# Performance work log

Measured on AMD Instinct MI355X. Metric: run time of the kernel, lower is better.

Reference implementation:

```python
import jax, jax.numpy as jnp
import numpy as np


def kernel_mus(n_kernels):
    l_mu = [1.0]
    if n_kernels == 1:
        return l_mu
    bin_size = 2.0 / (n_kernels - 1)
    l_mu.append(1 - bin_size / 2)
    for i in range(1, n_kernels - 1):
        l_mu.append(l_mu[i] - bin_size)
    return l_mu


def kernel_sigmas(n_kernels):
    bin_size = 2.0 / (n_kernels - 1)
    l_sigma = [0.0001]
    if n_kernels == 1:
        return l_sigma
    l_sigma += [0.5 * bin_size] * (n_kernels - 1)
    return l_sigma


def setup_inputs() -> dict:
    key = jax.random.key(0)
    k0, k1, k2, k3 = jax.random.split(key, 4)
    B, Q, D, E, V, K = 256, 32, 512, 300, 100000, 11
    query_tokens = jax.random.randint(k0, (B, Q), 0, V)
    doc_tokens = jax.random.randint(k1, (B, D), 0, V)
    emb_table = jax.random.normal(k2, (V, E), jnp.float32) * 0.02
    dense_w = jax.random.uniform(k3, (1, K), jnp.float32, -0.014, 0.014)
    dense_b = jnp.zeros((1,), jnp.float32)
    mu = jnp.asarray(kernel_mus(K), jnp.float32)
    sigma = jnp.asarray(kernel_sigmas(K), jnp.float32)
    return {"query_tokens": query_tokens, "doc_tokens": doc_tokens,
            "emb_table": emb_table, "dense_w": dense_w, "dense_b": dense_b,
            "mu": mu, "sigma": sigma}


def reference(query_tokens, doc_tokens, emb_table, dense_w, dense_b, mu, sigma):
    EPS = 1e-13  # CosineMatrixAttention tiny value
    q_mask = (query_tokens > 0).astype(jnp.float32)   # [B,Q]
    d_mask = (doc_tokens > 0).astype(jnp.float32)     # [B,D]
    q_emb = emb_table[query_tokens]                   # [B,Q,E]
    d_emb = emb_table[doc_tokens]                     # [B,D,E]
    q_n = q_emb / (jnp.linalg.norm(q_emb, axis=-1, keepdims=True) + EPS)
    d_n = d_emb / (jnp.linalg.norm(d_emb, axis=-1, keepdims=True) + EPS)
    cosine = jnp.einsum('bqe,bde->bqd', q_n, d_n)     # [B,Q,D]
    pair_mask = q_mask[:, :, None] * d_mask[:, None, :]  # [B,Q,D]
    cosine_masked = cosine * pair_mask
    # gaussian kernels: [B,Q,D,K]
    diff = cosine_masked[..., None] - mu
    kernels = jnp.exp(-(diff * diff) / (2.0 * sigma * sigma)) * pair_mask[..., None]
    per_kernel_query = jnp.sum(kernels, axis=2)       # [B,Q,K]
    log_pkq = jnp.log(jnp.clip(per_kernel_query, 1e-10)) * 0.01
    log_pkq = log_pkq * q_mask[..., None]
    per_kernel = jnp.sum(log_pkq, axis=1)             # [B,K]
    out = per_kernel @ dense_w.T + dense_b            # [B,1]
    return out[:, 0]
```

## Files before the change

### kernel.cpp

```cpp
#include <hip/hip_runtime.h>


#define B      256
#define BQ     32
#define BD     512
#define EDIM   300
#define KPAD   320
#define NK     11
#define DTILE  64
#define NCHUNK 16
#define DSTR   324

typedef float floatx4 __attribute__((ext_vector_type(4)));
typedef short shortx8 __attribute__((ext_vector_type(8)));

__device__ __forceinline__ unsigned short f2bf(float f) {
    unsigned int u = __float_as_uint(f);
    return (unsigned short)((u + 0x7fffu + ((u >> 16) & 1u)) >> 16);
}
__device__ __forceinline__ float bf2f(unsigned short h) {
    return __uint_as_float(((unsigned int)h) << 16);
}

__global__ __launch_bounds__(256)
void knrm_norm(const float* __restrict__ emb, unsigned short* __restrict__ ebf,
               float* __restrict__ rnorm, int V)
{
    int r    = blockIdx.x * 16 + (threadIdx.x >> 4);
    int part = threadIdx.x & 15;
    if (r >= V) return;
    const float4* src = (const float4*)(emb + (size_t)r * EDIM);
    uint2*        dst = (uint2*)(ebf + (size_t)r * KPAD);
    float ss = 0.f;
    #pragma unroll
    for (int i = 0; i < 5; ++i) {
        int c = part + i * 16;
        uint2 p = {0u, 0u};
        if (c < EDIM / 4) {
            float4 v = src[c];
            unsigned short h0 = f2bf(v.x), h1 = f2bf(v.y), h2 = f2bf(v.z), h3 = f2bf(v.w);
            p.x = (unsigned int)h0 | ((unsigned int)h1 << 16);
            p.y = (unsigned int)h2 | ((unsigned int)h3 << 16);
            float f0 = bf2f(h0), f1 = bf2f(h1), f2 = bf2f(h2), f3 = bf2f(h3);
            ss += f0 * f0 + f1 * f1 + f2 * f2 + f3 * f3;
        }
        dst[c] = p;
    }
    ss += __shfl_xor(ss, 1);
    ss += __shfl_xor(ss, 2);
    ss += __shfl_xor(ss, 4);
    ss += __shfl_xor(ss, 8);
    if (part == 0) rnorm[r] = 1.f / (sqrtf(ss) + 1e-13f);
}

__global__ __launch_bounds__(256)
void knrm_main3(const int* __restrict__ qtok, const int* __restrict__ dtok,
                const unsigned short* __restrict__ ebf, const float* __restrict__ rnorm,
                const float* __restrict__ mu, const float* __restrict__ sigma,
                float* __restrict__ pkq_part)
{
    __shared__ unsigned short d_buf[DTILE * DSTR];

    const int tid   = threadIdx.x;
    const int lane  = tid & 63;
    const int wv    = tid >> 6;
    const int b     = blockIdx.x >> 3;
    const int g     = blockIdx.x & 7;
    const int l16   = lane & 15;
    const int quad  = lane >> 4;
    const int mbase = (wv & 1) * 16;
    const int sub   = wv >> 1;
    const int nbase = sub * 32;
    const int chunk = g * 2 + sub;

    const int tq  = qtok[b * BQ + mbase + l16];
    const int td0 = dtok[b * BD + g * DTILE + nbase + l16];
    const int td1 = dtok[b * BD + g * DTILE + nbase + 16 + l16];
    float rq  = rnorm[tq];
    float rd0 = rnorm[td0], dm0 = (td0 > 0) ? 1.f : 0.f;
    float rd1 = rnorm[td1], dm1 = (td1 > 0) ? 1.f : 0.f;

    const uint4* asrc = (const uint4*)(ebf + (size_t)tq * KPAD);
    shortx8 afrag[10];
    #pragma unroll
    for (int ks = 0; ks < 10; ++ks)
        afrag[ks] = *(const shortx8*)&asrc[quad + ks * 4];

    float mur[NK], cfr[NK];
    #pragma unroll
    for (int k = 0; k < NK; ++k) {
        float s = sigma[k];
        mur[k] = mu[k];
        cfr[k] = -0.5f / (s * s);
    }

    {
        int row = tid >> 2, part = tid & 3;
        int tok = dtok[b * BD + g * DTILE + row];
        const uint4* src = (const uint4*)(ebf + (size_t)tok * KPAD);
        #pragma unroll
        for (int i = 0; i < 10; ++i) {
            int c = part + i * 4;
            *(uint4*)&d_buf[row * DSTR + c * 8] = src[c];
        }
    }
    __syncthreads();

    const unsigned short* b0ptr = &d_buf[(nbase + l16) * DSTR + quad * 8];
    const unsigned short* b1ptr = b0ptr + 16 * DSTR;

    floatx4 acc0 = {0.f, 0.f, 0.f, 0.f};
    floatx4 acc1 = {0.f, 0.f, 0.f, 0.f};
    #pragma unroll
    for (int ks = 0; ks < 10; ++ks) {
        shortx8 b0 = *(const shortx8*)(b0ptr + ks * 32);
        shortx8 b1 = *(const shortx8*)(b1ptr + ks * 32);
        acc0 = __builtin_amdgcn_mfma_f32_16x16x32_bf16(afrag[ks], b0, acc0, 0, 0, 0);
        acc1 = __builtin_amdgcn_mfma_f32_16x16x32_bf16(afrag[ks], b1, acc1, 0, 0, 0);
    }

    float rqv[4];
    #pragma unroll
    for (int r = 0; r < 4; ++r) rqv[r] = __shfl(rq, quad * 4 + r);

    float* dst = pkq_part + (size_t)(b * NCHUNK + chunk) * (BQ * NK);
    #pragma unroll
    for (int r = 0; r < 4; ++r) {
        float c0 = acc0[r] * rqv[r] * rd0;
        float c1 = acc1[r] * rqv[r] * rd1;
        int q = mbase + quad * 4 + r;
        #pragma unroll
        for (int k = 0; k < NK; ++k) {
            float d0 = c0 - mur[k];
            float d1 = c1 - mur[k];
            float v = dm0 * __expf(cfr[k] * d0 * d0)
                    + dm1 * __expf(cfr[k] * d1 * d1);
            v += __shfl_xor(v, 1);
            v += __shfl_xor(v, 2);
            v += __shfl_xor(v, 4);
            v += __shfl_xor(v, 8);
            if (l16 == 0) dst[q * NK + k] = v;
        }
    }
}

__global__ __launch_bounds__(64)
void knrm_epi(const int* __restrict__ qtok, const float* __restrict__ dw,
              const float* __restrict__ db, const float* __restrict__ pkq_part,
              float* __restrict__ out)
{
    int b = blockIdx.x, lane = threadIdx.x;
    float sq = 0.f;
    if (lane < BQ) {
        int tok = qtok[b * BQ + lane];
        if (tok > 0) {
            #pragma unroll
            for (int k = 0; k < NK; ++k) {
                float s = 0.f;
                #pragma unroll
                for (int c = 0; c < NCHUNK; ++c)
                    s += pkq_part[((size_t)(b * NCHUNK + c) * BQ + lane) * NK + k];
                sq += __logf(fmaxf(s, 1e-10f)) * 0.01f * dw[k];
            }
        }
    }
    sq += __shfl_xor(sq, 1);
    sq += __shfl_xor(sq, 2);
    sq += __shfl_xor(sq, 4);
    sq += __shfl_xor(sq, 8);
    sq += __shfl_xor(sq, 16);
    sq += __shfl_xor(sq, 32);
    if (lane == 0) out[b] = sq + db[0];
}

extern "C" void kernel_launch(void* const* d_in, const int* in_sizes, int n_in,
                              void* d_out, int out_size, void* d_ws, size_t ws_size,
                              hipStream_t stream)
{
    const int*   qtok  = (const int*)d_in[0];
    const int*   dtok  = (const int*)d_in[1];
    const float* emb   = (const float*)d_in[2];
    const float* dw    = (const float*)d_in[3];
    const float* dbias = (const float*)d_in[4];
    const float* mu    = (const float*)d_in[5];
    const float* sg    = (const float*)d_in[6];
    float* out = (float*)d_out;

    const int V = in_sizes[2] / EDIM;
    const size_t ebf_bytes = (size_t)V * KPAD * 2;
    const size_t rn_bytes  = (size_t)V * 4;

    unsigned short* ebf = (unsigned short*)d_ws;
    float* rnorm        = (float*)((char*)d_ws + ebf_bytes);
    float* pkq_part     = (float*)((char*)d_ws + ebf_bytes + rn_bytes);

    knrm_norm<<<(V + 15) / 16, 256, 0, stream>>>(emb, ebf, rnorm, V);
    knrm_main3<<<B * 8, 256, 0, stream>>>(qtok, dtok, ebf, rnorm, mu, sg, pkq_part);
    knrm_epi<<<B, 64, 0, stream>>>(qtok, dw, dbias, pkq_part, out);
}
```

Baseline: 250.8 us.

## Halve doc tile per block, doubling grid and partial-sum count

Each block now handles 32 document tokens instead of 64, so the main kernel launches twice as many blocks. Every wave computes a single 16x16 MFMA tile and one set of Gaussian kernels rather than two. Block ordering now puts the batch index in the low bits, and the LDS row stride changes to 328. The goal is more parallelism and occupancy (launch bounds request 5 blocks per CU). The trade-off is that each query embedding fragment is reloaded twice as often, and the epilogue must sum 32 partials instead of 16.

```diff
diff --git a/kernel.cpp b/kernel.cpp
--- a/kernel.cpp
+++ b/kernel.cpp
@@ -7,9 +7,9 @@
 #define EDIM   300
 #define KPAD   320
 #define NK     11
-#define DTILE  64
-#define NCHUNK 16
-#define DSTR   324
+#define DTILE  32
+#define NSEMI  32
+#define DSTR   328
 
 typedef float floatx4 __attribute__((ext_vector_type(4)));
 typedef short shortx8 __attribute__((ext_vector_type(8)));
@@ -53,8 +53,8 @@
     if (part == 0) rnorm[r] = 1.f / (sqrtf(ss) + 1e-13f);
 }
 
-__global__ __launch_bounds__(256)
-void knrm_main3(const int* __restrict__ qtok, const int* __restrict__ dtok,
+__global__ __launch_bounds__(256, 5)
+void knrm_main4(const int* __restrict__ qtok, const int* __restrict__ dtok,
                 const unsigned short* __restrict__ ebf, const float* __restrict__ rnorm,
                 const float* __restrict__ mu, const float* __restrict__ sigma,
                 float* __restrict__ pkq_part)
@@ -64,21 +64,19 @@
     const int tid   = threadIdx.x;
     const int lane  = tid & 63;
     const int wv    = tid >> 6;
-    const int b     = blockIdx.x >> 3;
-    const int g     = blockIdx.x & 7;
+    const int b     = blockIdx.x & 255;
+    const int chunk = blockIdx.x >> 8;
     const int l16   = lane & 15;
     const int quad  = lane >> 4;
     const int mbase = (wv & 1) * 16;
-    const int sub   = wv >> 1;
-    const int nbase = sub * 32;
-    const int chunk = g * 2 + sub;
+    const int nbase = (wv >> 1) * 16;
+    const int dbase = chunk * DTILE;
 
-    const int tq  = qtok[b * BQ + mbase + l16];
-    const int td0 = dtok[b * BD + g * DTILE + nbase + l16];
-    const int td1 = dtok[b * BD + g * DTILE + nbase + 16 + l16];
-    float rq  = rnorm[tq];
-    float rd0 = rnorm[td0], dm0 = (td0 > 0) ? 1.f : 0.f;
-    float rd1 = rnorm[td1], dm1 = (td1 > 0) ? 1.f : 0.f;
+    const int tq = qtok[b * BQ + mbase + l16];
+    const int td = dtok[b * BD + dbase + nbase + l16];
+    float rq = rnorm[tq];
+    float rd = rnorm[td];
+    float dm = (td > 0) ? 1.f : 0.f;
 
     const uint4* asrc = (const uint4*)(ebf + (size_t)tq * KPAD);
     shortx8 afrag[10];
@@ -95,46 +93,39 @@
     }
 
     {
-        int row = tid >> 2, part = tid & 3;
-        int tok = dtok[b * BD + g * DTILE + row];
+        int row = tid >> 3, part = tid & 7;
+        int tok = dtok[b * BD + dbase + row];
         const uint4* src = (const uint4*)(ebf + (size_t)tok * KPAD);
         #pragma unroll
-        for (int i = 0; i < 10; ++i) {
-            int c = part + i * 4;
+        for (int i = 0; i < 5; ++i) {
+            int c = part + i * 8;
             *(uint4*)&d_buf[row * DSTR + c * 8] = src[c];
         }
     }
     __syncthreads();
 
-    const unsigned short* b0ptr = &d_buf[(nbase + l16) * DSTR + quad * 8];
-    const unsigned short* b1ptr = b0ptr + 16 * DSTR;
-
-    floatx4 acc0 = {0.f, 0.f, 0.f, 0.f};
-    floatx4 acc1 = {0.f, 0.f, 0.f, 0.f};
+    const unsigned short* bptr = &d_buf[(nbase + l16) * DSTR + quad * 8];
+    floatx4 acc = {0.f, 0.f, 0.f, 0.f};
     #pragma unroll
     for (int ks = 0; ks < 10; ++ks) {
-        shortx8 b0 = *(const shortx8*)(b0ptr + ks * 32);
-        shortx8 b1 = *(const shortx8*)(b1ptr + ks * 32);
-        acc0 = __builtin_amdgcn_mfma_f32_16x16x32_bf16(afrag[ks], b0, acc0, 0, 0, 0);
-        acc1 = __builtin_amdgcn_mfma_f32_16x16x32_bf16(afrag[ks], b1, acc1, 0, 0, 0);
+        shortx8 bf = *(const shortx8*)(bptr + ks * 32);
+        acc = __builtin_amdgcn_mfma_f32_16x16x32_bf16(afrag[ks], bf, acc, 0, 0, 0);
     }
 
     float rqv[4];
     #pragma unroll
     for (int r = 0; r < 4; ++r) rqv[r] = __shfl(rq, quad * 4 + r);
 
-    float* dst = pkq_part + (size_t)(b * NCHUNK + chunk) * (BQ * NK);
+    const int semi = chunk * 2 + (nbase >> 4);
+    float* dst = pkq_part + (size_t)(b * NSEMI + semi) * (BQ * NK);
     #pragma unroll
     for (int r = 0; r < 4; ++r) {
-        float c0 = acc0[r] * rqv[r] * rd0;
-        float c1 = acc1[r] * rqv[r] * rd1;
+        float c0 = acc[r] * rqv[r] * rd;
         int q = mbase + quad * 4 + r;
         #pragma unroll
         for (int k = 0; k < NK; ++k) {
             float d0 = c0 - mur[k];
-            float d1 = c1 - mur[k];
-            float v = dm0 * __expf(cfr[k] * d0 * d0)
-                    + dm1 * __expf(cfr[k] * d1 * d1);
+            float v = dm * __expf(cfr[k] * d0 * d0);
             v += __shfl_xor(v, 1);
             v += __shfl_xor(v, 2);
             v += __shfl_xor(v, 4);
@@ -158,8 +149,8 @@
             for (int k = 0; k < NK; ++k) {
                 float s = 0.f;
                 #pragma unroll
-                for (int c = 0; c < NCHUNK; ++c)
-                    s += pkq_part[((size_t)(b * NCHUNK + c) * BQ + lane) * NK + k];
+                for (int c = 0; c < NSEMI; ++c)
+                    s += pkq_part[((size_t)(b * NSEMI + c) * BQ + lane) * NK + k];
                 sq += __logf(fmaxf(s, 1e-10f)) * 0.01f * dw[k];
             }
         }
@@ -195,6 +186,6 @@
     float* pkq_part     = (float*)((char*)d_ws + ebf_bytes + rn_bytes);
 
     knrm_norm<<<(V + 15) / 16, 256, 0, stream>>>(emb, ebf, rnorm, V);
-    knrm_main3<<<B * 8, 256, 0, stream>>>(qtok, dtok, ebf, rnorm, mu, sg, pkq_part);
+    knrm_main4<<<B * 16, 256, 0, stream>>>(qtok, dtok, ebf, rnorm, mu, sg, pkq_part);
     knrm_epi<<<B, 64, 0, stream>>>(qtok, dw, dbias, pkq_part, out);
 }
```

New measurement: 247.3 us. No clear change (-1.4%).
